# Kernel optimization log

Hardware: AMD Instinct MI355X
Metric: run time of the kernel (lower is better)

Reference implementation:

```python
import jax, jax.numpy as jnp
import numpy as np

DIM = 1024
HEADS = 16
HEAD_DIM = DIM // HEADS
SCALE = HEAD_DIM ** -0.5


def setup_inputs() -> dict:
    key = jax.random.key(0)
    k1, k2, k3, k4 = jax.random.split(key, 4)
    x = jax.random.normal(k1, (8, 1024, DIM), dtype=jnp.float32)
    # qkv: Linear(dim, 3*dim), bias=False; proj: Linear(dim, dim) with bias
    w_qkv = jax.random.normal(k2, (DIM, 3 * DIM), dtype=jnp.float32) * (DIM ** -0.5)
    w_proj = jax.random.normal(k3, (DIM, DIM), dtype=jnp.float32) * (DIM ** -0.5)
    b_proj = jax.random.normal(k4, (DIM,), dtype=jnp.float32) * 0.02
    return {"x": x, "w_qkv": w_qkv, "w_proj": w_proj, "b_proj": b_proj}


def reference(x, w_qkv, w_proj, b_proj):
    b, n, dim = x.shape
    h, d = HEADS, HEAD_DIM
    qkv = x @ w_qkv                                  # [b, n, 3*dim]
    qkv = qkv.reshape(b, n, 3, h, d)                  # split (qkv h d)
    q = jnp.transpose(qkv[:, :, 0], (0, 2, 1, 3))     # [b, h, n, d]
    k = jnp.transpose(qkv[:, :, 1], (0, 2, 1, 3))
    v = jnp.transpose(qkv[:, :, 2], (0, 2, 1, 3))
    dots = jnp.einsum('bhid,bhjd->bhij', q, k) * SCALE
    attn = jax.nn.softmax(dots, axis=-1)              # [b, h, n, n]
    out = jnp.einsum('bhij,bhjd->bhid', attn, v)      # [b, h, n, d]
    out = jnp.transpose(out, (0, 2, 1, 3)).reshape(b, n, dim)
    return out @ w_proj + b_proj
```

## Files before the change

### kernel.cpp

```cpp
#include <hip/hip_runtime.h>
#include <hip/hip_bf16.h>
#include <stdint.h>


typedef __attribute__((ext_vector_type(8))) short  short8;
typedef __attribute__((ext_vector_type(4))) float  floatx4;

#define MFMA_BF16(a, b, c) __builtin_amdgcn_mfma_f32_16x16x32_bf16((a), (b), (c), 0, 0, 0)

__device__ __forceinline__ uint16_t f2b(float f) {
    uint32_t i; __builtin_memcpy(&i, &f, 4);
    uint32_t r = i + 0x7FFFu + ((i >> 16) & 1u);
    return (uint16_t)(r >> 16);
}

#if defined(__has_builtin)
#if __has_builtin(__builtin_amdgcn_cvt_pk_bf16_f32)
#define HAVE_PK_BF16 1
#endif
#if __has_builtin(__builtin_amdgcn_exp2f)
#define EXP2F __builtin_amdgcn_exp2f
#endif
#endif
#ifndef EXP2F
#define EXP2F exp2f
#endif

__device__ __forceinline__ uint32_t pk_bf16(float a, float b) {
#ifdef HAVE_PK_BF16
    typedef __attribute__((ext_vector_type(2))) __bf16 bf16x2;
    bf16x2 v = __builtin_amdgcn_cvt_pk_bf16_f32(a, b);
    uint32_t u; __builtin_memcpy(&u, &v, 4); return u;
#else
    return (uint32_t)f2b(a) | ((uint32_t)f2b(b) << 16);
#endif
}

__device__ __forceinline__ void p32swap(uint32_t& a, uint32_t& b) {
    asm("v_permlane32_swap_b32 %0, %1" : "+v"(a), "+v"(b));
}
__device__ __forceinline__ void p16swap(uint32_t& a, uint32_t& b) {
    asm("v_permlane16_swap_b32 %0, %1" : "+v"(a), "+v"(b));
}

__device__ __forceinline__ void async16(uint16_t* lds, const uint16_t* g) {
    __builtin_amdgcn_global_load_lds(
        (const __attribute__((address_space(1))) uint32_t*)g,
        (__attribute__((address_space(3))) uint32_t*)lds,
        16, 0, 0);
}

__global__ __launch_bounds__(256) void cvt_f32_bf16(
    const float* __restrict__ in, uint16_t* __restrict__ out, int n4)
{
    const int i = blockIdx.x * 256 + threadIdx.x;
    if (i < n4) {
        const float4 v = ((const float4*)in)[i];
        ushort4 o;
        o.x = f2b(v.x); o.y = f2b(v.y); o.z = f2b(v.z); o.w = f2b(v.w);
        ((ushort4*)out)[i] = o;
    }
}

__global__ __launch_bounds__(256) void transpose_k(
    const float* __restrict__ in, uint16_t* __restrict__ out, int R, int C)
{
    __shared__ uint16_t t[32][33];
    const int bx = blockIdx.x * 32;
    const int by = blockIdx.y * 32;
    const int tx = threadIdx.x & 31, ty = threadIdx.x >> 5;
    #pragma unroll
    for (int j = 0; j < 32; j += 8)
        t[ty + j][tx] = f2b(in[(size_t)(by + ty + j) * C + bx + tx]);
    __syncthreads();
    #pragma unroll
    for (int j = 0; j < 32; j += 8)
        out[(size_t)(bx + ty + j) * R + by + tx] = t[tx][ty + j];
}

template <int EPI>
__global__ __launch_bounds__(256, 2) void gemm_bt(
    const uint16_t* __restrict__ A, const uint16_t* __restrict__ Bt,
    uint16_t* __restrict__ C, float* __restrict__ Cf,
    const float* __restrict__ bias, int M, int N, int K)
{
    __shared__ uint16_t As[128 * 64];
    __shared__ uint16_t Bs[128 * 64];

    const int tid  = threadIdx.x;
    const int lane = tid & 63, quad = lane >> 4, l16 = lane & 15;
    const int wv   = tid >> 6;
    const int wm   = (wv >> 1) * 64, wn = (wv & 1) * 64;

    const int lid = blockIdx.y * gridDim.x + blockIdx.x;
    const int nxl = gridDim.x >> 3;
    const int xcd = lid & 7, loc = lid >> 3;
    const int bx  = xcd * nxl + (loc % nxl);
    const int by  = loc / nxl;
    const int tm  = by * 128, tn = bx * 128;

    floatx4 acc[4][4] = {};

    for (int kt = 0; kt < K; kt += 64) {
        __syncthreads();
        #pragma unroll
        for (int i = 0; i < 4; i++) {
            const int li  = i * 256 + tid;
            const int row = li >> 3;
            const int cg  = (li & 7) ^ (row & 7);
            async16(&As[li * 8], &A[(size_t)(tm + row) * K + kt + cg * 8]);
        }
        #pragma unroll
        for (int i = 0; i < 4; i++) {
            const int li  = i * 256 + tid;
            const int row = li >> 3;
            const int cg  = (li & 7) ^ (row & 7);
            async16(&Bs[li * 8], &Bt[(size_t)(tn + row) * K + kt + cg * 8]);
        }
        __syncthreads();
        #pragma unroll
        for (int kc = 0; kc < 2; kc++) {
            short8 af[4], bf[4];
            #pragma unroll
            for (int mb = 0; mb < 4; mb++) {
                const int row = wm + mb * 16 + l16;
                const int g   = kc * 4 + quad;
                af[mb] = *(const short8*)&As[row * 64 + ((g ^ (row & 7)) * 8)];
            }
            #pragma unroll
            for (int nb = 0; nb < 4; nb++) {
                const int row = wn + nb * 16 + l16;
                const int g   = kc * 4 + quad;
                bf[nb] = *(const short8*)&Bs[row * 64 + ((g ^ (row & 7)) * 8)];
            }
            #pragma unroll
            for (int mb = 0; mb < 4; mb++)
                #pragma unroll
                for (int nb = 0; nb < 4; nb++)
                    acc[mb][nb] = MFMA_BF16(af[mb], bf[nb], acc[mb][nb]);
        }
    }

    if (EPI == 0) {
        const int which = (tn + wn) >> 10;
        if (which == 2) {
            #pragma unroll
            for (int nb = 0; nb < 4; nb++) {
                const int col = tn + wn + nb * 16 + l16;
                const int hh = (col >> 6) & 15, dd = col & 63;
                #pragma unroll
                for (int mb = 0; mb < 4; mb++) {
                    const int gm = tm + wm + mb * 16 + quad * 4;
                    const int b  = gm >> 10, n = gm & 1023;
                    const size_t rgn = (size_t)(256 + b * 16 + hh) * 65536;
                    uint2 o;
                    o.x = pk_bf16(acc[mb][nb][0], acc[mb][nb][1]);
                    o.y = pk_bf16(acc[mb][nb][2], acc[mb][nb][3]);
                    *(uint2*)&C[rgn + (size_t)dd * 1024 + n] = o;
                }
            }
        } else {
            const float qs = (which == 0) ? 0.18033688011112043f : 1.0f;
            #pragma unroll
            for (int nb = 0; nb < 4; nb++) {
                const int col = tn + wn + nb * 16 + l16;
                const int hh = (col >> 6) & 15, dd = col & 63;
                #pragma unroll
                for (int mb = 0; mb < 4; mb++)
                    #pragma unroll
                    for (int r = 0; r < 4; r++) {
                        const int gm = tm + wm + mb * 16 + quad * 4 + r;
                        const int b  = gm >> 10, n = gm & 1023;
                        const size_t rgn = (size_t)(which * 128 + b * 16 + hh) * 65536;
                        C[rgn + (size_t)n * 64 + dd] = f2b(acc[mb][nb][r] * qs);
                    }
            }
        }
    } else {
        #pragma unroll
        for (int nb = 0; nb < 4; nb++) {
            const int col = tn + wn + nb * 16 + l16;
            const float bv = bias[col];
            #pragma unroll
            for (int mb = 0; mb < 4; mb++)
                #pragma unroll
                for (int r = 0; r < 4; r++) {
                    const int gm = tm + wm + mb * 16 + quad * 4 + r;
                    Cf[(size_t)gm * N + col] = acc[mb][nb][r] + bv;
                }
        }
    }
}

__global__ __launch_bounds__(256, 4) void attn_fa(
    const uint16_t* __restrict__ qkv, uint16_t* __restrict__ out)
{
    __shared__ uint16_t Ks[2][64 * 64];
    __shared__ uint16_t Vs[2][64 * 64];

    const int tid  = threadIdx.x;
    const int lane = tid & 63, quad = lane >> 4, l16 = lane & 15;
    const int wv   = tid >> 6;
    const int bh   = blockIdx.x;
    const int q0   = blockIdx.y * 128 + wv * 32;

    const size_t qbase  = (size_t)bh * 65536;
    const size_t kbase  = (size_t)(128 + bh) * 65536;
    const size_t vtbase = (size_t)(256 + bh) * 65536;

    short8 qf[2][2];
    #pragma unroll
    for (int nq = 0; nq < 2; nq++)
        #pragma unroll
        for (int ks = 0; ks < 2; ks++)
            qf[nq][ks] = *(const short8*)&qkv[qbase + (size_t)(q0 + nq * 16 + l16) * 64 + ks * 32 + quad * 8];
    asm volatile("s_waitcnt vmcnt(0)" ::: "memory");

    short8 ones;
    #pragma unroll
    for (int j = 0; j < 8; j++) ones[j] = (short)0x3F80;

    const int li0 = tid,        r0 = li0 >> 3, c0 = (li0 & 7) ^ (r0 & 7);
    const int li1 = 256 + tid,  r1 = li1 >> 3, c1 = (li1 & 7) ^ (r1 & 7);
    const uint16_t* kg0 = &qkv[kbase + (size_t)r0 * 64 + c0 * 8];
    const uint16_t* kg1 = &qkv[kbase + (size_t)r1 * 64 + c1 * 8];
    const uint16_t* vg0 = &qkv[vtbase + (size_t)r0 * 1024 + c0 * 8];
    const uint16_t* vg1 = &qkv[vtbase + (size_t)r1 * 1024 + c1 * 8];

    floatx4 Oacc[2][4] = {};
    floatx4 Lacc[2] = {};

    #pragma unroll
    for (int pb = 0; pb < 2; pb++) {
        async16(&Ks[pb][li0 * 8], kg0 + pb * 4096);
        async16(&Ks[pb][li1 * 8], kg1 + pb * 4096);
        async16(&Vs[pb][li0 * 8], vg0 + pb * 64);
        async16(&Vs[pb][li1 * 8], vg1 + pb * 64);
    }
    const uint16_t* sk0 = kg0 + 2 * 4096;
    const uint16_t* sk1 = kg1 + 2 * 4096;
    const uint16_t* sv0 = vg0 + 2 * 64;
    const uint16_t* sv1 = vg1 + 2 * 64;
    __builtin_amdgcn_sched_barrier(0);
    asm volatile("s_waitcnt vmcnt(4)" ::: "memory");
    __builtin_amdgcn_s_barrier();

    for (int kb = 0; kb < 16; kb++) {
        const uint16_t* Kc = &Ks[kb & 1][0];
        const uint16_t* Vc = &Vs[kb & 1][0];

        short8 pf[2][2];
        #pragma unroll
        for (int kk = 0; kk < 2; kk++) {
            floatx4 st[2][2];
            #pragma unroll
            for (int mb2 = 0; mb2 < 2; mb2++) {
                const int krow = (kk * 2 + mb2) * 16 + l16;
                short8 kf0 = *(const short8*)&Kc[krow * 64 + ((quad ^ (krow & 7)) * 8)];
                short8 kf1 = *(const short8*)&Kc[krow * 64 + (((4 + quad) ^ (krow & 7)) * 8)];
                #pragma unroll
                for (int nq = 0; nq < 2; nq++) {
                    floatx4 z = {};
                    z = MFMA_BF16(kf0, qf[nq][0], z);
                    z = MFMA_BF16(kf1, qf[nq][1], z);
                    st[mb2][nq] = z;
                }
            }
            #pragma unroll
            for (int nq = 0; nq < 2; nq++) {
                uint32_t w0 = pk_bf16(EXP2F(st[0][nq][0]), EXP2F(st[0][nq][1]));
                uint32_t w1 = pk_bf16(EXP2F(st[0][nq][2]), EXP2F(st[0][nq][3]));
                uint32_t w2 = pk_bf16(EXP2F(st[1][nq][0]), EXP2F(st[1][nq][1]));
                uint32_t w3 = pk_bf16(EXP2F(st[1][nq][2]), EXP2F(st[1][nq][3]));
                p32swap(w0, w2); p16swap(w0, w2);
                p32swap(w1, w3); p16swap(w1, w3);
                uint32_t w[4] = { w0, w1, w2, w3 };
                __builtin_memcpy(&pf[nq][kk], w, 16);
            }
            #pragma unroll
            for (int qb = 0; qb < 2; qb++)
                Lacc[qb] = MFMA_BF16(pf[qb][kk], ones, Lacc[qb]);
        }
        #pragma unroll
        for (int nb = 0; nb < 4; nb++)
            #pragma unroll
            for (int kk = 0; kk < 2; kk++) {
                const int vrow = nb * 16 + l16;
                const int g    = kk * 4 + quad;
                short8 vf = *(const short8*)&Vc[vrow * 64 + ((g ^ (vrow & 7)) * 8)];
                #pragma unroll
                for (int qb = 0; qb < 2; qb++)
                    Oacc[qb][nb] = MFMA_BF16(pf[qb][kk], vf, Oacc[qb][nb]);
            }

        __builtin_amdgcn_sched_barrier(0);
        __builtin_amdgcn_s_barrier();
        if (kb + 2 < 16) {
            uint16_t* Kd = &Ks[kb & 1][0];
            uint16_t* Vd = &Vs[kb & 1][0];
            async16(&Kd[li0 * 8], sk0);  sk0 += 4096;
            async16(&Kd[li1 * 8], sk1);  sk1 += 4096;
            async16(&Vd[li0 * 8], sv0);  sv0 += 64;
            async16(&Vd[li1 * 8], sv1);  sv1 += 64;
            __builtin_amdgcn_sched_barrier(0);
            asm volatile("s_waitcnt vmcnt(4)" ::: "memory");
        } else {
            __builtin_amdgcn_sched_barrier(0);
            asm volatile("s_waitcnt vmcnt(0)" ::: "memory");
        }
        __builtin_amdgcn_s_barrier();
        __builtin_amdgcn_sched_barrier(0);
    }

    float inv[2][4];
    #pragma unroll
    for (int qb = 0; qb < 2; qb++)
        #pragma unroll
        for (int r = 0; r < 4; r++)
            inv[qb][r] = 1.f / Lacc[qb][r];

    const int b = bh >> 4, hh = bh & 15;
    #pragma unroll
    for (int qb = 0; qb < 2; qb++)
        #pragma unroll
        for (int nb = 0; nb < 4; nb++)
            #pragma unroll
            for (int r = 0; r < 4; r++) {
                const int n = q0 + qb * 16 + quad * 4 + r;
                out[((size_t)(b * 1024 + n)) * 1024 + hh * 64 + nb * 16 + l16] =
                    f2b(Oacc[qb][nb][r] * inv[qb][r]);
            }
}

extern "C" void kernel_launch(void* const* d_in, const int* in_sizes, int n_in,
                              void* d_out, int out_size, void* d_ws, size_t ws_size,
                              hipStream_t stream)
{
    const float* x      = (const float*)d_in[0];
    const float* w_qkv  = (const float*)d_in[1];
    const float* w_proj = (const float*)d_in[2];
    const float* b_proj = (const float*)d_in[3];
    float* out = (float*)d_out;

    uint16_t* ws   = (uint16_t*)d_ws;
    uint16_t* xb   = ws;
    uint16_t* wTq  = xb  + 8192 * 1024;
    uint16_t* wTp  = wTq + 3072 * 1024;
    uint16_t* qkvb = wTp + 1024 * 1024;
    uint16_t* ao   = xb;

    cvt_f32_bf16<<<8192, 256, 0, stream>>>(x, xb, 8192 * 1024 / 4);
    transpose_k<<<dim3(96, 32), 256, 0, stream>>>(w_qkv, wTq, 1024, 3072);
    transpose_k<<<dim3(32, 32), 256, 0, stream>>>(w_proj, wTp, 1024, 1024);
    gemm_bt<0><<<dim3(24, 64), 256, 0, stream>>>(xb, wTq, qkvb, nullptr, nullptr, 8192, 3072, 1024);
    attn_fa<<<dim3(128, 8), 256, 0, stream>>>(qkvb, ao);
    gemm_bt<1><<<dim3(8, 64), 256, 0, stream>>>(ao, wTp, nullptr, out, b_proj, 8192, 1024, 1024);
}
```

Measured before the change: 221.4 us.

## Double-buffer GEMM shared-memory tiles with async prefetch two tiles ahead

Makes the bf16 GEMM's LDS tiles double-buffered and issues async global-to-LDS loads for tile t+2 while computing tile t, using explicit vmcnt waits and barriers. This targets the exposed global load latency that the previous load-sync-compute loop paid on every k-step. LDS use doubles to 64 KB per block, which may limit occupancy under launch_bounds(256,2). The hand-written waitcnt counting must match the number of async loads issued.

```diff
diff --git a/kernel.cpp b/kernel.cpp
--- a/kernel.cpp
+++ b/kernel.cpp
@@ -84,8 +84,8 @@
     uint16_t* __restrict__ C, float* __restrict__ Cf,
     const float* __restrict__ bias, int M, int N, int K)
 {
-    __shared__ uint16_t As[128 * 64];
-    __shared__ uint16_t Bs[128 * 64];
+    __shared__ uint16_t As[2][128 * 64];
+    __shared__ uint16_t Bs[2][128 * 64];
 
     const int tid  = threadIdx.x;
     const int lane = tid & 63, quad = lane >> 4, l16 = lane & 15;
@@ -99,25 +99,38 @@
     const int by  = loc / nxl;
     const int tm  = by * 128, tn = bx * 128;
 
+    const int nt = K >> 6;
+
     floatx4 acc[4][4] = {};
 
-    for (int kt = 0; kt < K; kt += 64) {
-        __syncthreads();
-        #pragma unroll
-        for (int i = 0; i < 4; i++) {
-            const int li  = i * 256 + tid;
-            const int row = li >> 3;
-            const int cg  = (li & 7) ^ (row & 7);
-            async16(&As[li * 8], &A[(size_t)(tm + row) * K + kt + cg * 8]);
-        }
-        #pragma unroll
-        for (int i = 0; i < 4; i++) {
-            const int li  = i * 256 + tid;
-            const int row = li >> 3;
-            const int cg  = (li & 7) ^ (row & 7);
-            async16(&Bs[li * 8], &Bt[(size_t)(tn + row) * K + kt + cg * 8]);
-        }
-        __syncthreads();
+    #define STAGE_TILE(buf, kt)                                                  \
+        do {                                                                     \
+            _Pragma("unroll")                                                    \
+            for (int i = 0; i < 4; i++) {                                        \
+                const int li  = i * 256 + tid;                                   \
+                const int row = li >> 3;                                         \
+                const int cg  = (li & 7) ^ (row & 7);                            \
+                async16(&As[buf][li * 8], &A[(size_t)(tm + row) * K + (kt) + cg * 8]); \
+            }                                                                    \
+            _Pragma("unroll")                                                    \
+            for (int i = 0; i < 4; i++) {                                        \
+                const int li  = i * 256 + tid;                                   \
+                const int row = li >> 3;                                         \
+                const int cg  = (li & 7) ^ (row & 7);                            \
+                async16(&Bs[buf][li * 8], &Bt[(size_t)(tn + row) * K + (kt) + cg * 8]); \
+            }                                                                    \
+        } while (0)
+
+    STAGE_TILE(0, 0);
+    STAGE_TILE(1, 64);
+    __builtin_amdgcn_sched_barrier(0);
+    asm volatile("s_waitcnt vmcnt(8)" ::: "memory");
+    __builtin_amdgcn_s_barrier();
+
+    for (int t = 0; t < nt; t++) {
+        const int cur = t & 1;
+        const uint16_t* Ac = &As[cur][0];
+        const uint16_t* Bc = &Bs[cur][0];
         #pragma unroll
         for (int kc = 0; kc < 2; kc++) {
             short8 af[4], bf[4];
@@ -125,13 +138,13 @@
             for (int mb = 0; mb < 4; mb++) {
                 const int row = wm + mb * 16 + l16;
                 const int g   = kc * 4 + quad;
-                af[mb] = *(const short8*)&As[row * 64 + ((g ^ (row & 7)) * 8)];
+                af[mb] = *(const short8*)&Ac[row * 64 + ((g ^ (row & 7)) * 8)];
             }
             #pragma unroll
             for (int nb = 0; nb < 4; nb++) {
                 const int row = wn + nb * 16 + l16;
                 const int g   = kc * 4 + quad;
-                bf[nb] = *(const short8*)&Bs[row * 64 + ((g ^ (row & 7)) * 8)];
+                bf[nb] = *(const short8*)&Bc[row * 64 + ((g ^ (row & 7)) * 8)];
             }
             #pragma unroll
             for (int mb = 0; mb < 4; mb++)
@@ -139,7 +152,20 @@
                 for (int nb = 0; nb < 4; nb++)
                     acc[mb][nb] = MFMA_BF16(af[mb], bf[nb], acc[mb][nb]);
         }
-    }
+        __builtin_amdgcn_sched_barrier(0);
+        __builtin_amdgcn_s_barrier();
+        if (t + 2 < nt) {
+            STAGE_TILE(cur, (t + 2) << 6);
+            __builtin_amdgcn_sched_barrier(0);
+            asm volatile("s_waitcnt vmcnt(8)" ::: "memory");
+        } else {
+            __builtin_amdgcn_sched_barrier(0);
+            asm volatile("s_waitcnt vmcnt(0)" ::: "memory");
+        }
+        __builtin_amdgcn_s_barrier();
+        __builtin_amdgcn_sched_barrier(0);
+    }
+    #undef STAGE_TILE
 
     if (EPI == 0) {
         const int which = (tn + wn) >> 10;
```

After: 238.1 us. 1.08x slower.
